# Optimization experiments

Measured on AMD Instinct MI355X. Metric: run time of the kernel, lower is better.

## Reference

```python
import jax, jax.numpy as jnp
import numpy as np

FEATS_DIM = 64
N_CELLS = 50000
N_GENES = 20000
N_EDGES = 3000000


def setup_inputs() -> dict:
    key = jax.random.key(0)
    ks = jax.random.split(key, 12)
    c_feat = jax.random.normal(ks[0], (N_CELLS, FEATS_DIM), dtype=jnp.float32)
    g_feat = jax.random.normal(ks[1], (N_GENES, FEATS_DIM), dtype=jnp.float32)
    cs_factor = jax.random.uniform(ks[2], (N_CELLS, 1), dtype=jnp.float32)
    gs_factor = jax.random.uniform(ks[3], (N_GENES, 1), dtype=jnp.float32)
    edge_u = jax.random.randint(ks[4], (N_EDGES,), 0, N_CELLS, dtype=jnp.int32)
    edge_v = jax.random.randint(ks[5], (N_EDGES,), 0, N_GENES, dtype=jnp.int32)
    s = 1.0 / np.sqrt(FEATS_DIM)
    W_mean = jax.random.uniform(ks[6], (FEATS_DIM, 1), jnp.float32, -s, s)
    b_mean = jax.random.uniform(ks[7], (1,), jnp.float32, -s, s)
    W_disp = jax.random.uniform(ks[8], (FEATS_DIM, 1), jnp.float32, -s, s)
    b_disp = jax.random.uniform(ks[9], (1,), jnp.float32, -s, s)
    W_pi = jax.random.uniform(ks[10], (FEATS_DIM, 1), jnp.float32, -s, s)
    b_pi = jax.random.uniform(ks[11], (1,), jnp.float32, -s, s)
    return {
        "c_feat": c_feat, "g_feat": g_feat,
        "cs_factor": cs_factor, "gs_factor": gs_factor,
        "edge_u": edge_u, "edge_v": edge_v,
        "W_mean": W_mean, "b_mean": b_mean,
        "W_disp": W_disp, "b_disp": b_disp,
        "W_pi": W_pi, "b_pi": b_pi,
    }


def reference(c_feat, g_feat, cs_factor, gs_factor, edge_u, edge_v,
              W_mean, b_mean, W_disp, b_disp, W_pi, b_pi):
    # edge gather: h_d[e] = c_feat[src(e)] * g_feat[dst(e)]  -> [E, d]
    h_d = c_feat[edge_u] * g_feat[edge_v]
    # per-edge factors gathered from node data -> [E, 1]
    gs_e = gs_factor[edge_v]
    cs_e = cs_factor[edge_u]
    # tiny d->1 linears
    mu_ = jax.nn.sigmoid(h_d @ W_mean + b_mean)      # dec_mean
    disp_ = h_d @ W_disp + b_disp                     # dec_disp
    pi = jax.nn.sigmoid(h_d @ W_pi + b_pi)            # dec_pi
    # DispAct: clamp(softplus(x), 1e-4, 1e4)
    disp = jnp.clip(jax.nn.softplus(gs_e * disp_), 1e-4, 1e4)
    # MeanAct: clamp(exp(x)-1, 1e-5, 1e6)
    mu = cs_e * jnp.clip(jnp.exp(gs_e * mu_) - 1.0, 1e-5, 1e6)
    return (mu, disp, pi)
```

## Files before the change

### kernel.cpp

```cpp
#include <hip/hip_runtime.h>
#include <math.h>


typedef _Float16 h2 __attribute__((ext_vector_type(2)));

#if __has_builtin(__builtin_amdgcn_fdot2)
__device__ __forceinline__ float fdot2f(h2 a, h2 b, float c) {
    return __builtin_amdgcn_fdot2(a, b, c, false);
}
#else
__device__ __forceinline__ float fdot2f(h2 a, h2 b, float c) {
    return fmaf((float)a.x, (float)b.x, fmaf((float)a.y, (float)b.y, c));
}
#endif

__device__ __forceinline__ float red8(float x) {
#if __has_builtin(__builtin_amdgcn_mov_dpp) && __has_builtin(__builtin_amdgcn_ds_swizzle)
    int t;
    t = __builtin_amdgcn_mov_dpp(__float_as_int(x), 0xB1, 0xF, 0xF, 1);
    x += __int_as_float(t);
    t = __builtin_amdgcn_mov_dpp(__float_as_int(x), 0x4E, 0xF, 0xF, 1);
    x += __int_as_float(t);
    t = __builtin_amdgcn_ds_swizzle(__float_as_int(x), 0x101F);
    x += __int_as_float(t);
#else
    x += __shfl_xor(x, 1);
    x += __shfl_xor(x, 2);
    x += __shfl_xor(x, 4);
#endif
    return x;
}

__device__ __forceinline__ unsigned pack2h(float lo, float hi) {
    h2 p = {(_Float16)lo, (_Float16)hi};
    return __builtin_bit_cast(unsigned, p);
}

__global__ __launch_bounds__(256) void zinb_pack_kernel(
    const float4* __restrict__ c_src, const float4* __restrict__ g_src,
    uint4* __restrict__ c_dst, uint4* __restrict__ g_dst,
    int n_c_groups, int n_total_groups)
{
    const int i = (int)(blockIdx.x * blockDim.x + threadIdx.x);
    if (i >= n_total_groups) return;
    const float4* src; uint4* dst; int j;
    if (i < n_c_groups) { src = c_src; dst = c_dst; j = i; }
    else                { src = g_src; dst = g_dst; j = i - n_c_groups; }
    const float4 a = src[2 * j];
    const float4 b = src[2 * j + 1];
    uint4 o;
    o.x = pack2h(a.x, a.y);
    o.y = pack2h(a.z, a.w);
    o.z = pack2h(b.x, b.y);
    o.w = pack2h(b.z, b.w);
    dst[j] = o;
}

__global__ __launch_bounds__(256) void zinb_edge_f16_kernel(
    const uint4* __restrict__ c_pack,
    const uint4* __restrict__ g_pack,
    const float* __restrict__ cs_factor,
    const float* __restrict__ gs_factor,
    const int* __restrict__ edge_u,
    const int* __restrict__ edge_v,
    const float* __restrict__ W_mean, const float* __restrict__ b_mean,
    const float* __restrict__ W_disp, const float* __restrict__ b_disp,
    const float* __restrict__ W_pi,   const float* __restrict__ b_pi,
    float* __restrict__ out_mu,
    float* __restrict__ out_disp,
    float* __restrict__ out_pi,
    int n_edges)
{
    const int lane = (int)(threadIdx.x & 63);
    const int k    = lane & 7;
    const int grp  = lane >> 3;

    h2 wm[4], wd[4], wp[4];
    #pragma unroll
    for (int i = 0; i < 4; ++i) {
        wm[i] = (h2){(_Float16)W_mean[8 * k + 2 * i], (_Float16)W_mean[8 * k + 2 * i + 1]};
        wd[i] = (h2){(_Float16)W_disp[8 * k + 2 * i], (_Float16)W_disp[8 * k + 2 * i + 1]};
        wp[i] = (h2){(_Float16)W_pi  [8 * k + 2 * i], (_Float16)W_pi  [8 * k + 2 * i + 1]};
    }
    const float bm = b_mean[0], bd = b_disp[0], bp = b_pi[0];

    const int perm = (k << 3) | grp;

    int e0 = (int)(blockIdx.x * blockDim.x + threadIdx.x) & ~63;
    const int stride = (int)(gridDim.x * blockDim.x);

    for (; e0 < n_edges; e0 += stride) {
        const int et  = e0 + perm;
        const int etc = (et < n_edges) ? et : (n_edges - 1);
        const int ut = edge_u[etc];
        const int vt = edge_v[etc];
        const float cs_t = cs_factor[ut];
        const float gs_t = gs_factor[vt];

        float pmk = 0.f, pdk = 0.f, ppk = 0.f;

        #pragma unroll
        for (int j = 0; j < 8; ++j) {
            int ej = e0 + 8 * j + grp;
            if (ej >= n_edges) ej = n_edges - 1;
            const int u = edge_u[ej];
            const int v = edge_v[ej];
            const uint4 cu4 = c_pack[(size_t)u * 8 + k];
            const uint4 gu4 = g_pack[(size_t)v * 8 + k];

            const h2 c0 = __builtin_bit_cast(h2, cu4.x), g0 = __builtin_bit_cast(h2, gu4.x);
            const h2 c1 = __builtin_bit_cast(h2, cu4.y), g1 = __builtin_bit_cast(h2, gu4.y);
            const h2 c2 = __builtin_bit_cast(h2, cu4.z), g2 = __builtin_bit_cast(h2, gu4.z);
            const h2 c3 = __builtin_bit_cast(h2, cu4.w), g3 = __builtin_bit_cast(h2, gu4.w);
            const h2 h0 = c0 * g0;
            const h2 h1 = c1 * g1;
            const h2 hh2 = c2 * g2;
            const h2 h3 = c3 * g3;

            float pm = 0.f, pd = 0.f, pp = 0.f;
            pm = fdot2f(h0, wm[0], pm); pm = fdot2f(h1, wm[1], pm);
            pm = fdot2f(hh2, wm[2], pm); pm = fdot2f(h3, wm[3], pm);
            pd = fdot2f(h0, wd[0], pd); pd = fdot2f(h1, wd[1], pd);
            pd = fdot2f(hh2, wd[2], pd); pd = fdot2f(h3, wd[3], pd);
            pp = fdot2f(h0, wp[0], pp); pp = fdot2f(h1, wp[1], pp);
            pp = fdot2f(hh2, wp[2], pp); pp = fdot2f(h3, wp[3], pp);

            pm = red8(pm);
            pd = red8(pd);
            pp = red8(pp);

            if (k == j) { pmk = pm; pdk = pd; ppk = pp; }
        }

        const float mu_ = __builtin_amdgcn_rcpf(1.f + __expf(-(pmk + bm)));
        const float pi_ = __builtin_amdgcn_rcpf(1.f + __expf(-(ppk + bp)));

        const float sx = gs_t * (pdk + bd);
        const float sp = fmaxf(sx, 0.f) + __logf(1.f + __expf(-fabsf(sx)));
        const float disp = fminf(fmaxf(sp, 1e-4f), 1e4f);

        const float mu = cs_t * fminf(fmaxf(__expf(gs_t * mu_) - 1.f, 1e-5f), 1e6f);

        if (et < n_edges) {
            __builtin_nontemporal_store(mu,   out_mu + et);
            __builtin_nontemporal_store(disp, out_disp + et);
            __builtin_nontemporal_store(pi_,  out_pi + et);
        }
    }
}

__global__ __launch_bounds__(256) void zinb_edge_f32_kernel(
    const float* __restrict__ c_feat,
    const float* __restrict__ g_feat,
    const float* __restrict__ cs_factor,
    const float* __restrict__ gs_factor,
    const int* __restrict__ edge_u,
    const int* __restrict__ edge_v,
    const float* __restrict__ W_mean, const float* __restrict__ b_mean,
    const float* __restrict__ W_disp, const float* __restrict__ b_disp,
    const float* __restrict__ W_pi,   const float* __restrict__ b_pi,
    float* __restrict__ out_mu,
    float* __restrict__ out_disp,
    float* __restrict__ out_pi,
    int n_edges)
{
    __shared__ float4 wlds[48];
    {
        const int t = threadIdx.x;
        if (t < 48) {
            const int which = t / 16;
            const int kk    = t % 16;
            const float4* src = (which == 0) ? (const float4*)W_mean
                              : (which == 1) ? (const float4*)W_disp
                                             : (const float4*)W_pi;
            wlds[kk * 3 + which] = src[kk];
        }
    }
    __syncthreads();

    const float bm = b_mean[0], bd = b_disp[0], bp = b_pi[0];
    const float4* __restrict__ c4 = (const float4*)c_feat;
    const float4* __restrict__ g4 = (const float4*)g_feat;

    const int tid    = (int)(blockIdx.x * blockDim.x + threadIdx.x);
    const int stride = (int)(gridDim.x * blockDim.x);

    for (int e = tid; e < n_edges; e += stride) {
        const int u = edge_u[e];
        const int v = edge_v[e];
        const float4* __restrict__ cb = c4 + (size_t)u * 16;
        const float4* __restrict__ gb = g4 + (size_t)v * 16;

        float pm = 0.f, pd = 0.f, pp = 0.f;
        #pragma unroll
        for (int kk = 0; kk < 16; ++kk) {
            const float4 cc = cb[kk];
            const float4 gg = gb[kk];
            const float4 wmv = wlds[kk * 3 + 0];
            const float4 wdv = wlds[kk * 3 + 1];
            const float4 wpv = wlds[kk * 3 + 2];
            const float hx = cc.x * gg.x;
            const float hy = cc.y * gg.y;
            const float hz = cc.z * gg.z;
            const float hw = cc.w * gg.w;
            pm = fmaf(hx, wmv.x, fmaf(hy, wmv.y, fmaf(hz, wmv.z, fmaf(hw, wmv.w, pm))));
            pd = fmaf(hx, wdv.x, fmaf(hy, wdv.y, fmaf(hz, wdv.z, fmaf(hw, wdv.w, pd))));
            pp = fmaf(hx, wpv.x, fmaf(hy, wpv.y, fmaf(hz, wpv.z, fmaf(hw, wpv.w, pp))));
        }

        const float gs = gs_factor[v];
        const float cs = cs_factor[u];
        const float mu_ = __builtin_amdgcn_rcpf(1.f + __expf(-(pm + bm)));
        const float pi_ = __builtin_amdgcn_rcpf(1.f + __expf(-(pp + bp)));
        const float sx = gs * (pd + bd);
        const float sp = fmaxf(sx, 0.f) + __logf(1.f + __expf(-fabsf(sx)));
        const float disp = fminf(fmaxf(sp, 1e-4f), 1e4f);
        const float mu = cs * fminf(fmaxf(__expf(gs * mu_) - 1.f, 1e-5f), 1e6f);

        out_mu[e]   = mu;
        out_disp[e] = disp;
        out_pi[e]   = pi_;
    }
}

extern "C" void kernel_launch(void* const* d_in, const int* in_sizes, int n_in,
                              void* d_out, int out_size, void* d_ws, size_t ws_size,
                              hipStream_t stream) {
    const float* c_feat = (const float*)d_in[0];
    const float* g_feat = (const float*)d_in[1];
    const float* cs     = (const float*)d_in[2];
    const float* gs     = (const float*)d_in[3];
    const int*   eu     = (const int*)d_in[4];
    const int*   ev     = (const int*)d_in[5];
    const float* Wm     = (const float*)d_in[6];
    const float* bm     = (const float*)d_in[7];
    const float* Wd     = (const float*)d_in[8];
    const float* bd     = (const float*)d_in[9];
    const float* Wp     = (const float*)d_in[10];
    const float* bp     = (const float*)d_in[11];

    const int E       = in_sizes[4];
    const int n_cells = in_sizes[0] / 64;
    const int n_genes = in_sizes[1] / 64;

    float* out_mu   = (float*)d_out;
    float* out_disp = out_mu + E;
    float* out_pi   = out_mu + 2 * (size_t)E;

    const size_t c_bytes = (size_t)n_cells * 64 * 2;
    const size_t g_bytes = (size_t)n_genes * 64 * 2;

    if (ws_size >= c_bytes + g_bytes) {
        uint4* c_pack = (uint4*)d_ws;
        uint4* g_pack = (uint4*)((char*)d_ws + c_bytes);

        const int n_c_groups = n_cells * 8;
        const int n_total    = n_c_groups + n_genes * 8;
        dim3 pgrid((n_total + 255) / 256), pblock(256);
        hipLaunchKernelGGL(zinb_pack_kernel, pgrid, pblock, 0, stream,
                           (const float4*)c_feat, (const float4*)g_feat,
                           c_pack, g_pack, n_c_groups, n_total);

        dim3 grid(2048), block(256);
        hipLaunchKernelGGL(zinb_edge_f16_kernel, grid, block, 0, stream,
                           c_pack, g_pack, cs, gs, eu, ev,
                           Wm, bm, Wd, bd, Wp, bp,
                           out_mu, out_disp, out_pi, E);
    } else {
        dim3 grid(2048), block(256);
        hipLaunchKernelGGL(zinb_edge_f32_kernel, grid, block, 0, stream,
                           c_feat, g_feat, cs, gs, eu, ev,
                           Wm, bm, Wd, bd, Wp, bp,
                           out_mu, out_disp, out_pi, E);
    }
}
```

Before: 185.8 us.

## Prefetch next edge's packed rows, use DPP row_shr reduce, raise occupancy hint

The inner 8-edge loop now loads the next iteration's packed cell and gene rows before computing the current one, a software prefetch meant to hide gather latency. The ds_swizzle step in the 8-lane reduction is replaced with a DPP move, which avoids an LDS-path instruction. The launch bounds now request 8 blocks per CU, which caps register use. In a fully unrolled loop the compiler may already have scheduled these loads early, and the register cap could cause spills. The third DPP control (0x141, a row_shr of 1 under the documented DPP encoding) looks like it may not produce the xor-4 partner, so the reduction could give wrong sums.

```diff
diff --git a/kernel.cpp b/kernel.cpp
--- a/kernel.cpp
+++ b/kernel.cpp
@@ -15,19 +15,13 @@
 #endif
 
 __device__ __forceinline__ float red8(float x) {
-#if __has_builtin(__builtin_amdgcn_mov_dpp) && __has_builtin(__builtin_amdgcn_ds_swizzle)
     int t;
-    t = __builtin_amdgcn_mov_dpp(__float_as_int(x), 0xB1, 0xF, 0xF, 1);
+    t = __builtin_amdgcn_mov_dpp(__float_as_int(x), 0xB1, 0xF, 0xF, true);
     x += __int_as_float(t);
-    t = __builtin_amdgcn_mov_dpp(__float_as_int(x), 0x4E, 0xF, 0xF, 1);
+    t = __builtin_amdgcn_mov_dpp(__float_as_int(x), 0x4E, 0xF, 0xF, true);
     x += __int_as_float(t);
-    t = __builtin_amdgcn_ds_swizzle(__float_as_int(x), 0x101F);
+    t = __builtin_amdgcn_mov_dpp(__float_as_int(x), 0x141, 0xF, 0xF, true);
     x += __int_as_float(t);
-#else
-    x += __shfl_xor(x, 1);
-    x += __shfl_xor(x, 2);
-    x += __shfl_xor(x, 4);
-#endif
     return x;
 }
 
@@ -56,7 +50,7 @@
     dst[j] = o;
 }
 
-__global__ __launch_bounds__(256) void zinb_edge_f16_kernel(
+__global__ __launch_bounds__(256, 8) void zinb_edge_f16_kernel(
     const uint4* __restrict__ c_pack,
     const uint4* __restrict__ g_pack,
     const float* __restrict__ cs_factor,
@@ -97,16 +91,22 @@
         const float cs_t = cs_factor[ut];
         const float gs_t = gs_factor[vt];
 
+        int ej0 = e0 + grp;
+        if (ej0 >= n_edges) ej0 = n_edges - 1;
+        uint4 cu4 = c_pack[(size_t)edge_u[ej0] * 8 + k];
+        uint4 gu4 = g_pack[(size_t)edge_v[ej0] * 8 + k];
+
         float pmk = 0.f, pdk = 0.f, ppk = 0.f;
 
         #pragma unroll
         for (int j = 0; j < 8; ++j) {
-            int ej = e0 + 8 * j + grp;
-            if (ej >= n_edges) ej = n_edges - 1;
-            const int u = edge_u[ej];
-            const int v = edge_v[ej];
-            const uint4 cu4 = c_pack[(size_t)u * 8 + k];
-            const uint4 gu4 = g_pack[(size_t)v * 8 + k];
+            uint4 ncu, ngu;
+            if (j < 7) {
+                int en = e0 + 8 * (j + 1) + grp;
+                if (en >= n_edges) en = n_edges - 1;
+                ncu = c_pack[(size_t)edge_u[en] * 8 + k];
+                ngu = g_pack[(size_t)edge_v[en] * 8 + k];
+            }
 
             const h2 c0 = __builtin_bit_cast(h2, cu4.x), g0 = __builtin_bit_cast(h2, gu4.x);
             const h2 c1 = __builtin_bit_cast(h2, cu4.y), g1 = __builtin_bit_cast(h2, gu4.y);
@@ -130,6 +130,8 @@
             pp = red8(pp);
 
             if (k == j) { pmk = pm; pdk = pd; ppk = pp; }
+
+            cu4 = ncu; gu4 = ngu;
         }
 
         const float mu_ = __builtin_amdgcn_rcpf(1.f + __expf(-(pmk + bm)));
```

Result: slower. 198.6 us (+6.9%).
